# Kernel tuning notes

Hardware: AMD Instinct MI355X
Metric: run time of the kernel (lower is better)

## Reference

```python
import jax, jax.numpy as jnp
import numpy as np

D_MODEL = 2048
N_HEAD = 16
HEAD_DIM = D_MODEL // N_HEAD
SCALE = 1.0 / (HEAD_DIM ** 0.5)


def setup_inputs() -> dict:
    key = jax.random.key(0)
    kx, kq, kk, kv, ko = jax.random.split(key, 5)
    std = 1.0 / np.sqrt(D_MODEL)
    return {
        "x": jax.random.normal(kx, (2, 2048, D_MODEL), dtype=jnp.float32),
        "w_q": jax.random.normal(kq, (D_MODEL, D_MODEL), dtype=jnp.float32) * std,
        "w_k": jax.random.normal(kk, (D_MODEL, D_MODEL), dtype=jnp.float32) * std,
        "w_v": jax.random.normal(kv, (D_MODEL, D_MODEL), dtype=jnp.float32) * std,
        "w_o": jax.random.normal(ko, (D_MODEL, D_MODEL), dtype=jnp.float32) * std,
    }


def reference(x, w_q, w_k, w_v, w_o):
    b, s, d = x.shape
    # nn.Linear(d,d,bias=False): y = x @ W^T, weights stored [out, in]
    def proj(w):
        y = jnp.einsum("bsd,ed->bse", x, w)
        return y.reshape(b, s, N_HEAD, HEAD_DIM).transpose(0, 2, 1, 3)  # [b,h,s,hd]
    q, k, v = proj(w_q), proj(w_k), proj(w_v)
    scores = jnp.einsum("bhqd,bhkd->bhqk", q, k) * SCALE  # [b,h,s,s]
    probs = jax.nn.softmax(scores, axis=-1)
    attn = jnp.einsum("bhqk,bhkd->bhqd", probs, v)
    attn = attn.transpose(0, 2, 1, 3).reshape(b, s, d)
    return jnp.einsum("bsd,ed->bse", attn, w_o)
```

## Files before the change

### kernel.cpp

```cpp
#include <hip/hip_runtime.h>

#define D_MODEL 2048
#define SEQ 2048
#define BATCH 2
#define NH 16
#define HD 128
#define MTOT 4096
#define NQKV 6144
#define QSTRIDE 4096

static constexpr float SCALE_LOG2E = 0.08838834764831845f * 1.4426950408889634f;

typedef __bf16 bf16x8 __attribute__((ext_vector_type(8)));
typedef _Float16 f16x4 __attribute__((ext_vector_type(4)));
typedef float f32x4 __attribute__((ext_vector_type(4)));

__device__ inline unsigned short f2bf(float f) {
  unsigned int u = __builtin_bit_cast(unsigned int, f);
  u += 0x7fffu + ((u >> 16) & 1u);
  return (unsigned short)(u >> 16);
}

__device__ inline float bf2f(unsigned int u) {
  return __builtin_bit_cast(float, u << 16);
}

__device__ inline float fast_exp2(float x) {
#if __has_builtin(__builtin_amdgcn_exp2f)
  return __builtin_amdgcn_exp2f(x);
#else
  return exp2f(x);
#endif
}

__device__ inline unsigned int bperm(int srcLane, unsigned int v) {
  return (unsigned int)__builtin_amdgcn_ds_bpermute(srcLane << 2, (int)v);
}

__device__ inline void gload_lds16(const void* g, void* s) {
  __builtin_amdgcn_global_load_lds(
      (__attribute__((address_space(1))) void*)g,
      (__attribute__((address_space(3))) void*)s, 16, 0, 0);
}

#define BARX() __builtin_amdgcn_s_barrier()
#define PRIO(x) __builtin_amdgcn_s_setprio(x)
#define LGK0()                                              \
  do {                                                      \
    asm volatile("s_waitcnt lgkmcnt(0)" ::: "memory");      \
    __builtin_amdgcn_sched_barrier(0);                      \
  } while (0)
#define VMW(n) asm volatile("s_waitcnt vmcnt(" #n ")" ::: "memory")

__global__ __launch_bounds__(256) void cvt_all(
    const float* __restrict__ x, const float* __restrict__ wq,
    const float* __restrict__ wk, const float* __restrict__ wv,
    const float* __restrict__ wo, unsigned short* __restrict__ xb,
    unsigned short* __restrict__ wqkv, unsigned short* __restrict__ wob) {
  const int y = blockIdx.y;
  const float* src;
  unsigned short* dst;
  int n4;
  if (y == 0) { src = x; dst = xb; n4 = MTOT * D_MODEL / 4; }
  else if (y == 4) { src = wo; dst = wob; n4 = D_MODEL * D_MODEL / 4; }
  else {
    src = (y == 1) ? wq : (y == 2) ? wk : wv;
    dst = wqkv + (size_t)(y - 1) * D_MODEL * D_MODEL;
    n4 = D_MODEL * D_MODEL / 4;
  }
  int i = blockIdx.x * 256 + threadIdx.x;
  if (i < n4) {
    float4 v = ((const float4*)src)[i];
    ushort4 o;
    o.x = f2bf(v.x); o.y = f2bf(v.y); o.z = f2bf(v.z); o.w = f2bf(v.w);
    ((ushort4*)dst)[i] = o;
  }
}

__global__ __launch_bounds__(512, 2) void gemm_qk(
    const unsigned short* __restrict__ A, const unsigned short* __restrict__ B,
    unsigned short* __restrict__ QK) {
  extern __shared__ __align__(16) char smem[];
  const int tid = threadIdx.x;
  const int lane = tid & 63;
  const int wave = tid >> 6;
  const int quad = lane >> 4;
  const int l15 = lane & 15;
  const int bid = blockIdx.x;
  const int wgid = (bid & 7) * 32 + (bid >> 3);
  const int tm = wgid >> 4, tn = wgid & 15;
  const int m0 = tm * 256, n0 = tn * 256;
  const int wm = wave >> 2;
  const int wn = wave & 3;

  const unsigned short* Ag = A + (size_t)(m0 + wave * 8 + (lane >> 3)) * 2048 +
                             (((lane & 7) ^ (lane >> 3)) * 8);
  const unsigned short* Bg = B + (size_t)(n0 + wave * 8 + (lane >> 3)) * 2048 +
                             (((lane & 7) ^ (lane >> 3)) * 8);
  char* sd = smem + wave * 1024;

  const int arow0 = (wm * 128 + l15) * 128;
  const int brow0 = (wn * 64 + l15) * 128;
  const int sk0 = (quad ^ (l15 & 7)) * 16;
  const int sk1 = ((4 + quad) ^ (l15 & 7)) * 16;

  f32x4 acc[8][4] = {};
  bf16x8 a[4][2], bl[2][2], bh[2][2];

#define QSA(u, nb, ko) \
  gload_lds16(Ag + (size_t)(u) * 64 * 2048 + (ko), sd + (nb) * 65536 + (u) * 8192)
#define QSB(u, nb, ko) \
  gload_lds16(Bg + (size_t)(u) * 64 * 2048 + (ko), sd + (nb) * 65536 + 32768 + (u) * 8192)
#define QRA(mh, cb)                                                               \
  _Pragma("unroll") for (int mi = 0; mi < 4; mi++) {                              \
    a[mi][0] = *(const bf16x8*)(smem + (cb) * 65536 + arow0 + ((mh) * 64 + mi * 16) * 128 + sk0); \
    a[mi][1] = *(const bf16x8*)(smem + (cb) * 65536 + arow0 + ((mh) * 64 + mi * 16) * 128 + sk1); \
  }
#define QRB(dst, nh, cb)                                                          \
  _Pragma("unroll") for (int ni = 0; ni < 2; ni++) {                              \
    dst[ni][0] = *(const bf16x8*)(smem + (cb) * 65536 + 32768 + brow0 + ((nh) * 32 + ni * 16) * 128 + sk0); \
    dst[ni][1] = *(const bf16x8*)(smem + (cb) * 65536 + 32768 + brow0 + ((nh) * 32 + ni * 16) * 128 + sk1); \
  }
#define QMM(mh, bsrc, nh)                                                         \
  _Pragma("unroll") for (int mi = 0; mi < 4; mi++)                                \
  _Pragma("unroll") for (int ni = 0; ni < 2; ni++) {                              \
    acc[(mh) * 4 + mi][(nh) * 2 + ni] = __builtin_amdgcn_mfma_f32_16x16x32_bf16(  \
        a[mi][0], bsrc[ni][0], acc[(mh) * 4 + mi][(nh) * 2 + ni], 0, 0, 0);       \
    acc[(mh) * 4 + mi][(nh) * 2 + ni] = __builtin_amdgcn_mfma_f32_16x16x32_bf16(  \
        a[mi][1], bsrc[ni][1], acc[(mh) * 4 + mi][(nh) * 2 + ni], 0, 0, 0);       \
  }

  QSB(0, 0, 0); QSB(1, 0, 0); QSB(2, 0, 0); QSB(3, 0, 0);
  QSA(0, 0, 0); QSA(2, 0, 0); QSA(1, 0, 0); QSA(3, 0, 0);
  VMW(0);
  BARX();

#define QKTILE(t, cb, nb)                                                         \
  {                                                                               \
    const int ko = (((t) + 1) & 31) * 64;                                         \
                                                                         \
    QRA(0, cb); QRB(bl, 0, cb);                                                   \
    QSB(0, nb, ko); QSB(1, nb, ko);                                               \
    BARX(); LGK0(); PRIO(1); QMM(0, bl, 0); PRIO(0); BARX();                      \
                                                                         \
    QRB(bh, 1, cb);                                                               \
    QSB(2, nb, ko); QSB(3, nb, ko);                                               \
    BARX(); LGK0(); PRIO(1); QMM(0, bh, 1); PRIO(0); VMW(4); BARX();              \
                                                                         \
    QRA(1, cb);                                                                   \
    QSA(0, nb, ko); QSA(2, nb, ko);                                               \
    BARX(); LGK0(); PRIO(1); QMM(1, bl, 0); PRIO(0); BARX();                      \
                                                                         \
    QSA(1, nb, ko); QSA(3, nb, ko);                                               \
    PRIO(1); QMM(1, bh, 1); PRIO(0); VMW(2); BARX();                              \
  }

  for (int t = 0; t < 32; t += 2) {
    QKTILE(t, 0, 1);
    QKTILE(t + 1, 1, 0);
  }

#pragma unroll
  for (int mi = 0; mi < 8; mi++)
#pragma unroll
    for (int ni = 0; ni < 4; ni++) {
      const int mm = m0 + wm * 128 + mi * 16 + quad * 4;
      const int nn = n0 + wn * 64 + ni * 16 + l15;
#pragma unroll
      for (int r = 0; r < 4; r++)
        QK[(size_t)(mm + r) * QSTRIDE + nn] = f2bf(acc[mi][ni][r]);
    }
#undef QSA
#undef QSB
#undef QRA
#undef QRB
#undef QMM
#undef QKTILE
}

#define VCORE_BODY(Aptr, Bptr)                                                    \
  const int tid = threadIdx.x;                                                    \
  const int lane = tid & 63;                                                      \
  const int wave = tid >> 6;                                                      \
  const int quad = lane >> 4;                                                     \
  const int l15 = lane & 15;                                                      \
  const int bid = blockIdx.x;                                                     \
  const int wgid = (bid & 7) * 32 + (bid >> 3);                                   \
  const int tm = wgid >> 3, tn = wgid & 7;                                        \
  const int m0 = tm * 128, n0 = tn * 256;                                         \
  const int wm = wave >> 1;                                             \
  const int wn = wave & 1;                                              \
  const unsigned short* Ag = (Aptr) + (size_t)(m0 + wave * 8 + (lane >> 3)) * 2048 + \
                             (((lane & 7) ^ (lane >> 3)) * 8);                    \
  const unsigned short* Bg = (Bptr) + (size_t)(n0 + wave * 8 + (lane >> 3)) * 2048 + \
                             (((lane & 7) ^ (lane >> 3)) * 8);                    \
  char* sd = smem + wave * 1024;                                                  \
  const int arow0 = (wm * 32 + l15) * 128;                                        \
  const int brow0 = (wn * 128 + l15) * 128;                                       \
  const int sk0 = (quad ^ (l15 & 7)) * 16;                                        \
  const int sk1 = ((4 + quad) ^ (l15 & 7)) * 16;                                  \
  f32x4 acc[2][8] = {};                                                           \
  bf16x8 a[2][2], bl[4][2], bh[4][2];

#define VSA(u, nb, ko) \
  gload_lds16(Ag + (size_t)(u) * 64 * 2048 + (ko), sd + (nb) * 49152 + (u) * 8192)
#define VSB(u, nb, ko) \
  gload_lds16(Bg + (size_t)(u) * 64 * 2048 + (ko), sd + (nb) * 49152 + 16384 + (u) * 8192)
#define VRA(cb)                                                                   \
  _Pragma("unroll") for (int mi = 0; mi < 2; mi++) {                              \
    a[mi][0] = *(const bf16x8*)(smem + (cb) * 49152 + arow0 + mi * 2048 + sk0);   \
    a[mi][1] = *(const bf16x8*)(smem + (cb) * 49152 + arow0 + mi * 2048 + sk1);   \
  }
#define VRB(dst, nh, cb)                                                          \
  _Pragma("unroll") for (int ni = 0; ni < 4; ni++) {                              \
    dst[ni][0] = *(const bf16x8*)(smem + (cb) * 49152 + 16384 + brow0 + ((nh) * 64 + ni * 16) * 128 + sk0); \
    dst[ni][1] = *(const bf16x8*)(smem + (cb) * 49152 + 16384 + brow0 + ((nh) * 64 + ni * 16) * 128 + sk1); \
  }
#define VMM(bsrc, nh)                                                             \
  _Pragma("unroll") for (int mi = 0; mi < 2; mi++)                                \
  _Pragma("unroll") for (int ni = 0; ni < 4; ni++) {                              \
    acc[mi][(nh) * 4 + ni] = __builtin_amdgcn_mfma_f32_16x16x32_bf16(             \
        a[mi][0], bsrc[ni][0], acc[mi][(nh) * 4 + ni], 0, 0, 0);                  \
    acc[mi][(nh) * 4 + ni] = __builtin_amdgcn_mfma_f32_16x16x32_bf16(             \
        a[mi][1], bsrc[ni][1], acc[mi][(nh) * 4 + ni], 0, 0, 0);                  \
  }
#define VSTAGE6(nb, ko)                                                           \
  VSA(0, nb, ko); VSA(1, nb, ko); VSB(0, nb, ko);                                 \
  VSB(1, nb, ko); VSB(2, nb, ko); VSB(3, nb, ko);

#define VTILE(t, cb, nb)                                                          \
  {                                                                               \
    const int ko = (((t) + 2) & 31) * 64;                                         \
                                                                         \
    VRA(cb); VRB(bl, 0, cb);                                                      \
    VSA(0, nb, ko); VSA(1, nb, ko); VSB(0, nb, ko);                               \
    BARX(); LGK0(); PRIO(1); VMM(bl, 0); PRIO(0); BARX();                         \
                                                                         \
    VRB(bh, 1, cb);                                                               \
    VSB(1, nb, ko); VSB(2, nb, ko); VSB(3, nb, ko);                               \
    BARX(); LGK0(); PRIO(1); VMM(bh, 1); PRIO(0); VMW(6); BARX();                 \
  }

#define VCORE_LOOP()                                                              \
  VSTAGE6(0, 0);                                                                  \
  VSTAGE6(1, 64);                                                                 \
  VMW(6);                                                                         \
  BARX();                                                                         \
  for (int t = 0; t < 30; t += 3) {                                               \
    VTILE(t + 0, 0, 2);                                                           \
    VTILE(t + 1, 1, 0);                                                           \
    VTILE(t + 2, 2, 1);                                                           \
  }                                                                               \
  VTILE(30, 0, 2);                                                                \
  VTILE(31, 1, 0);

__global__ __launch_bounds__(512, 2) void gemm_v(
    const unsigned short* __restrict__ A, const unsigned short* __restrict__ B,
    unsigned short* __restrict__ Vt) {
  extern __shared__ __align__(16) char smem[];
  VCORE_BODY(A, B);
  VCORE_LOOP();

  VMW(0);
  BARX();
  unsigned short* T = (unsigned short*)smem;
  const int h0 = n0 >> 7;
  const int bb = m0 >> 11;
  const int sbase = m0 & (SEQ - 1);
#pragma unroll
  for (int mi = 0; mi < 2; mi++)
#pragma unroll
    for (int q = 0; q < 8; q++) {
      const int d = q * 16 + l15;
      const int slocal = wm * 32 + mi * 16 + quad * 4;
      ushort4 hv;
      hv.x = f2bf(acc[mi][q][0]);
      hv.y = f2bf(acc[mi][q][1]);
      hv.z = f2bf(acc[mi][q][2]);
      hv.w = f2bf(acc[mi][q][3]);
      *(ushort4*)(T + wn * 17408 + d * 136 + slocal) = hv;
    }
  BARX();
  const int hd2 = tid >> 8;
  const int d = (tid >> 1) & 127;
  const int sc = (tid & 1) * 64;
  const size_t vrow = ((size_t)((bb * NH + h0 + hd2) * HD + d)) * SEQ + sbase + sc;
#pragma unroll
  for (int j = 0; j < 8; j++) {
    float4 c4 = *(const float4*)(T + hd2 * 17408 + d * 136 + sc + j * 8);
    *(float4*)(Vt + vrow + j * 8) = c4;
  }
}

__global__ __launch_bounds__(512, 2) void gemm_out(
    const unsigned short* __restrict__ A, const unsigned short* __restrict__ B,
    float* __restrict__ C) {
  extern __shared__ __align__(16) char smem[];
  VCORE_BODY(A, B);
  VCORE_LOOP();

#pragma unroll
  for (int mi = 0; mi < 2; mi++)
#pragma unroll
    for (int q = 0; q < 8; q++) {
      const int mm = m0 + wm * 32 + mi * 16 + quad * 4;
      const int nn = n0 + wn * 128 + q * 16 + l15;
#pragma unroll
      for (int r = 0; r < 4; r++)
        C[(size_t)(mm + r) * D_MODEL + nn] = acc[mi][q][r];
    }
}

__global__ __launch_bounds__(256, 2) void flash_attn(
    const unsigned short* __restrict__ QK, const unsigned short* __restrict__ Vt,
    unsigned short* __restrict__ Og) {
  __shared__ __align__(16) unsigned short Ks[2][64 * 128];
  const int tid = threadIdx.x;
  const int lane = tid & 63;
  const int wave = tid >> 6;
  const int quad = lane >> 4;
  const int l15 = lane & 15;
  const int id = blockIdx.x;
  const int xr = id & 7;
  const int kk = id >> 3;
  const int bh = xr * 4 + (kk >> 4);
  const int b = bh >> 4, h = bh & 15;
  const int q0 = (kk & 15) * 128;

  const size_t kbase = (size_t)(b * SEQ) * QSTRIDE + D_MODEL + h * HD;
  const size_t vbase = (size_t)bh * HD * SEQ;

  bf16x8 qf[2][4];
#pragma unroll
  for (int t = 0; t < 2; t++)
#pragma unroll
    for (int kc = 0; kc < 4; kc++)
      qf[t][kc] = *(const bf16x8*)(QK + (size_t)(b * SEQ + q0 + wave * 32 + t * 16 + l15) * QSTRIDE +
                                   h * HD + kc * 32 + quad * 8);

  const unsigned short* kg[4];
  int klofs[4];
#pragma unroll
  for (int i = 0; i < 4; i++) {
    int krow = wave * 16 + i * 4 + quad;
    int kc_ = l15 ^ (i * 4 + quad);
    kg[i] = QK + kbase + (size_t)krow * QSTRIDE + kc_ * 8;
    klofs[i] = (wave * 16 + i * 4) * 128;
  }

  const unsigned short* vp[8];
#pragma unroll
  for (int jt = 0; jt < 8; jt++)
    vp[jt] = Vt + vbase + (size_t)(jt * 16 + l15) * SEQ + quad * 8;

#pragma unroll
  for (int i = 0; i < 4; i++) gload_lds16(kg[i], &Ks[0][klofs[i]]);
#pragma unroll
  for (int i = 0; i < 4; i++) kg[i] += 64 * QSTRIDE;
  VMW(0);
  __syncthreads();

  float lsum[2] = {0.f, 0.f};
  f32x4 Oa[2][8] = {};

  const int laA = l15 + 32 * (quad & 1);
  const int laB = laA + 16;
  const bool hi = quad >= 2;

  for (int it = 0; it < SEQ / 64; ++it) {
    const int cur = it & 1;
    if (it < SEQ / 64 - 1) {
#pragma unroll
      for (int i = 0; i < 4; i++) gload_lds16(kg[i], &Ks[cur ^ 1][klofs[i]]);
#pragma unroll
      for (int i = 0; i < 4; i++) kg[i] += 64 * QSTRIDE;
    }

    const unsigned short* kb = &Ks[cur][0];
    f32x4 sacc[2][4] = {};
    PRIO(1);
#pragma unroll
    for (int js = 0; js < 4; js++)
#pragma unroll
      for (int kc = 0; kc < 4; kc++) {
        bf16x8 kf = *(const bf16x8*)(kb + (js * 16 + l15) * 128 + (((kc * 4 + quad) ^ l15) * 8));
        sacc[0][js] = __builtin_amdgcn_mfma_f32_16x16x32_bf16(kf, qf[0][kc], sacc[0][js], 0, 0, 0);
        sacc[1][js] = __builtin_amdgcn_mfma_f32_16x16x32_bf16(kf, qf[1][kc], sacc[1][js], 0, 0, 0);
      }
    PRIO(0);

    unsigned int pw[2][4][2];
#pragma unroll
    for (int t = 0; t < 2; t++)
#pragma unroll
      for (int js = 0; js < 4; js++) {
        float p0 = fast_exp2(sacc[t][js][0] * SCALE_LOG2E);
        float p1 = fast_exp2(sacc[t][js][1] * SCALE_LOG2E);
        float p2 = fast_exp2(sacc[t][js][2] * SCALE_LOG2E);
        float p3 = fast_exp2(sacc[t][js][3] * SCALE_LOG2E);
        unsigned int b0 = f2bf(p0), b1 = f2bf(p1), b2 = f2bf(p2), b3 = f2bf(p3);
        pw[t][js][0] = b0 | (b1 << 16);
        pw[t][js][1] = b2 | (b3 << 16);
        lsum[t] += (bf2f(b0) + bf2f(b1)) + (bf2f(b2) + bf2f(b3));
      }

    bf16x8 pb8[2][2];
#pragma unroll
    for (int t = 0; t < 2; t++)
#pragma unroll
      for (int g = 0; g < 2; g++) {
        const int j0 = 2 * g, j1 = 2 * g + 1;
        unsigned int a0 = bperm(laA, pw[t][j0][0]), c0 = bperm(laA, pw[t][j1][0]);
        unsigned int a1 = bperm(laA, pw[t][j0][1]), c1 = bperm(laA, pw[t][j1][1]);
        unsigned int a2 = bperm(laB, pw[t][j0][0]), c2 = bperm(laB, pw[t][j1][0]);
        unsigned int a3 = bperm(laB, pw[t][j0][1]), c3 = bperm(laB, pw[t][j1][1]);
        uint4 u;
        u.x = hi ? c0 : a0;
        u.y = hi ? c1 : a1;
        u.z = hi ? c2 : a2;
        u.w = hi ? c3 : a3;
        pb8[t][g] = __builtin_bit_cast(bf16x8, u);
      }

    const int ko = it * 64;
    PRIO(1);
#pragma unroll
    for (int jt = 0; jt < 8; jt++) {
      bf16x8 v0 = *(const bf16x8*)(vp[jt] + ko);
      bf16x8 v1 = *(const bf16x8*)(vp[jt] + ko + 32);
      Oa[0][jt] = __builtin_amdgcn_mfma_f32_16x16x32_bf16(v0, pb8[0][0], Oa[0][jt], 0, 0, 0);
      Oa[1][jt] = __builtin_amdgcn_mfma_f32_16x16x32_bf16(v0, pb8[1][0], Oa[1][jt], 0, 0, 0);
      Oa[0][jt] = __builtin_amdgcn_mfma_f32_16x16x32_bf16(v1, pb8[0][1], Oa[0][jt], 0, 0, 0);
      Oa[1][jt] = __builtin_amdgcn_mfma_f32_16x16x32_bf16(v1, pb8[1][1], Oa[1][jt], 0, 0, 0);
    }
    PRIO(0);

    if (it < SEQ / 64 - 1) {
      VMW(0);
    }
    __syncthreads();
  }

  float inv[2];
#pragma unroll
  for (int t = 0; t < 2; t++) {
    float s = lsum[t];
    s += __shfl_xor(s, 16);
    s += __shfl_xor(s, 32);
    inv[t] = 1.0f / s;
  }

#pragma unroll
  for (int t = 0; t < 2; t++) {
    const size_t rowbase = (size_t)(b * SEQ + q0 + wave * 32 + t * 16 + l15) * D_MODEL + h * HD;
#pragma unroll
    for (int jt = 0; jt < 8; jt++) {
      ushort4 o;
      o.x = f2bf(Oa[t][jt][0] * inv[t]);
      o.y = f2bf(Oa[t][jt][1] * inv[t]);
      o.z = f2bf(Oa[t][jt][2] * inv[t]);
      o.w = f2bf(Oa[t][jt][3] * inv[t]);
      *(ushort4*)(Og + rowbase + jt * 16 + quad * 4) = o;
    }
  }
}

extern "C" void kernel_launch(void* const* d_in, const int* in_sizes, int n_in,
                              void* d_out, int out_size, void* d_ws, size_t ws_size,
                              hipStream_t stream) {
  const float* x = (const float*)d_in[0];
  const float* wq = (const float*)d_in[1];
  const float* wk = (const float*)d_in[2];
  const float* wv = (const float*)d_in[3];
  const float* wo = (const float*)d_in[4];
  float* out = (float*)d_out;
  char* ws = (char*)d_ws;
  const size_t MB = 1u << 20;
  if (ws_size < 96 * MB) return;

  unsigned short* xb = (unsigned short*)(ws);
  unsigned short* wqkv = (unsigned short*)(ws + 16 * MB);
  unsigned short* wob = (unsigned short*)(ws + 40 * MB);
  unsigned short* QKb = (unsigned short*)(ws + 48 * MB);
  unsigned short* Vtb = (unsigned short*)(ws + 80 * MB);
  unsigned short* Ab = xb;

  static int lds_set = 0;
  if (!lds_set) {
    hipFuncSetAttribute((const void*)gemm_qk,
                        hipFuncAttributeMaxDynamicSharedMemorySize, 131072);
    hipFuncSetAttribute((const void*)gemm_v,
                        hipFuncAttributeMaxDynamicSharedMemorySize, 147456);
    hipFuncSetAttribute((const void*)gemm_out,
                        hipFuncAttributeMaxDynamicSharedMemorySize, 147456);
    lds_set = 1;
  }

  cvt_all<<<dim3(8192, 5), 256, 0, stream>>>(x, wq, wk, wv, wo, xb, wqkv, wob);

  gemm_qk<<<256, 512, 131072, stream>>>(xb, wqkv, QKb);
  gemm_v<<<256, 512, 147456, stream>>>(xb, wqkv + (size_t)4096 * 2048, Vtb);

  flash_attn<<<512, 256, 0, stream>>>(QKb, Vtb, Ab);

  gemm_out<<<256, 512, 147456, stream>>>(Ab, wob, out);
}
```

Measured before the change: 423.7 us.

## Stage V tiles through double-buffered swizzled LDS in flash attention

```diff
diff --git a/kernel.cpp b/kernel.cpp
--- a/kernel.cpp
+++ b/kernel.cpp
@@ -12,7 +12,6 @@
 static constexpr float SCALE_LOG2E = 0.08838834764831845f * 1.4426950408889634f;
 
 typedef __bf16 bf16x8 __attribute__((ext_vector_type(8)));
-typedef _Float16 f16x4 __attribute__((ext_vector_type(4)));
 typedef float f32x4 __attribute__((ext_vector_type(4)));
 
 __device__ inline unsigned short f2bf(float f) {
@@ -315,6 +314,7 @@
     const unsigned short* __restrict__ QK, const unsigned short* __restrict__ Vt,
     unsigned short* __restrict__ Og) {
   __shared__ __align__(16) unsigned short Ks[2][64 * 128];
+  __shared__ __align__(16) unsigned short Vs[2][128 * 64];
   const int tid = threadIdx.x;
   const int lane = tid & 63;
   const int wave = tid >> 6;
@@ -348,15 +348,25 @@
     klofs[i] = (wave * 16 + i * 4) * 128;
   }
 
-  const unsigned short* vp[8];
-#pragma unroll
-  for (int jt = 0; jt < 8; jt++)
-    vp[jt] = Vt + vbase + (size_t)(jt * 16 + l15) * SEQ + quad * 8;
+  const unsigned short* vg[4];
+  int vlofs[4];
+#pragma unroll
+  for (int u = 0; u < 4; u++) {
+    int vrow = u * 32 + (tid >> 3);
+    int vslot = tid & 7;
+    int vchunk = vslot ^ (vrow & 7);
+    vg[u] = Vt + vbase + (size_t)vrow * SEQ + vchunk * 8;
+    vlofs[u] = vrow * 64 + vslot * 8;
+  }
 
 #pragma unroll
   for (int i = 0; i < 4; i++) gload_lds16(kg[i], &Ks[0][klofs[i]]);
 #pragma unroll
+  for (int u = 0; u < 4; u++) gload_lds16(vg[u], &Vs[0][vlofs[u]]);
+#pragma unroll
   for (int i = 0; i < 4; i++) kg[i] += 64 * QSTRIDE;
+#pragma unroll
+  for (int u = 0; u < 4; u++) vg[u] += 64;
   VMW(0);
   __syncthreads();
 
@@ -366,6 +376,8 @@
   const int laA = l15 + 32 * (quad & 1);
   const int laB = laA + 16;
   const bool hi = quad >= 2;
+  const int vsk0 = (quad ^ (l15 & 7)) * 8;
+  const int vsk1 = ((4 + quad) ^ (l15 & 7)) * 8;
 
   for (int it = 0; it < SEQ / 64; ++it) {
     const int cur = it & 1;
@@ -373,7 +385,11 @@
 #pragma unroll
       for (int i = 0; i < 4; i++) gload_lds16(kg[i], &Ks[cur ^ 1][klofs[i]]);
 #pragma unroll
+      for (int u = 0; u < 4; u++) gload_lds16(vg[u], &Vs[cur ^ 1][vlofs[u]]);
+#pragma unroll
       for (int i = 0; i < 4; i++) kg[i] += 64 * QSTRIDE;
+#pragma unroll
+      for (int u = 0; u < 4; u++) vg[u] += 64;
     }
 
     const unsigned short* kb = &Ks[cur][0];
@@ -422,12 +438,13 @@
         pb8[t][g] = __builtin_bit_cast(bf16x8, u);
       }
 
-    const int ko = it * 64;
+    const unsigned short* vb = &Vs[cur][0];
     PRIO(1);
 #pragma unroll
     for (int jt = 0; jt < 8; jt++) {
-      bf16x8 v0 = *(const bf16x8*)(vp[jt] + ko);
-      bf16x8 v1 = *(const bf16x8*)(vp[jt] + ko + 32);
+      const int vrow = (jt * 16 + l15) * 64;
+      bf16x8 v0 = *(const bf16x8*)(vb + vrow + vsk0);
+      bf16x8 v1 = *(const bf16x8*)(vb + vrow + vsk1);
       Oa[0][jt] = __builtin_amdgcn_mfma_f32_16x16x32_bf16(v0, pb8[0][0], Oa[0][jt], 0, 0, 0);
       Oa[1][jt] = __builtin_amdgcn_mfma_f32_16x16x32_bf16(v0, pb8[1][0], Oa[1][jt], 0, 0, 0);
       Oa[0][jt] = __builtin_amdgcn_mfma_f32_16x16x32_bf16(v1, pb8[0][1], Oa[0][jt], 0, 0, 0);
```

After: 363.2 us. -14.3%, faster.

## Stage V tiles in LDS, use 8 waves per flash block, fold scale into Q

Applied to the files above, without the earlier changes.

```diff
diff --git a/kernel.cpp b/kernel.cpp
--- a/kernel.cpp
+++ b/kernel.cpp
@@ -12,17 +12,12 @@
 static constexpr float SCALE_LOG2E = 0.08838834764831845f * 1.4426950408889634f;
 
 typedef __bf16 bf16x8 __attribute__((ext_vector_type(8)));
-typedef _Float16 f16x4 __attribute__((ext_vector_type(4)));
 typedef float f32x4 __attribute__((ext_vector_type(4)));
 
 __device__ inline unsigned short f2bf(float f) {
   unsigned int u = __builtin_bit_cast(unsigned int, f);
   u += 0x7fffu + ((u >> 16) & 1u);
   return (unsigned short)(u >> 16);
-}
-
-__device__ inline float bf2f(unsigned int u) {
-  return __builtin_bit_cast(float, u << 16);
 }
 
 __device__ inline float fast_exp2(float x) {
@@ -160,6 +155,7 @@
     QKTILE(t + 1, 1, 0);
   }
 
+  const float qs = (n0 < 2048) ? SCALE_LOG2E : 1.0f;
 #pragma unroll
   for (int mi = 0; mi < 8; mi++)
 #pragma unroll
@@ -168,7 +164,7 @@
       const int nn = n0 + wn * 64 + ni * 16 + l15;
 #pragma unroll
       for (int r = 0; r < 4; r++)
-        QK[(size_t)(mm + r) * QSTRIDE + nn] = f2bf(acc[mi][ni][r]);
+        QK[(size_t)(mm + r) * QSTRIDE + nn] = f2bf(acc[mi][ni][r] * qs);
     }
 #undef QSA
 #undef QSB
@@ -311,10 +307,11 @@
     }
 }
 
-__global__ __launch_bounds__(256, 2) void flash_attn(
+__global__ __launch_bounds__(512, 4) void flash_attn(
     const unsigned short* __restrict__ QK, const unsigned short* __restrict__ Vt,
     unsigned short* __restrict__ Og) {
   __shared__ __align__(16) unsigned short Ks[2][64 * 128];
+  __shared__ __align__(16) unsigned short Vs[2][128 * 64];
   const int tid = threadIdx.x;
   const int lane = tid & 63;
   const int wave = tid >> 6;
@@ -330,108 +327,111 @@
   const size_t kbase = (size_t)(b * SEQ) * QSTRIDE + D_MODEL + h * HD;
   const size_t vbase = (size_t)bh * HD * SEQ;
 
-  bf16x8 qf[2][4];
-#pragma unroll
-  for (int t = 0; t < 2; t++)
-#pragma unroll
-    for (int kc = 0; kc < 4; kc++)
-      qf[t][kc] = *(const bf16x8*)(QK + (size_t)(b * SEQ + q0 + wave * 32 + t * 16 + l15) * QSTRIDE +
-                                   h * HD + kc * 32 + quad * 8);
-
-  const unsigned short* kg[4];
-  int klofs[4];
-#pragma unroll
-  for (int i = 0; i < 4; i++) {
-    int krow = wave * 16 + i * 4 + quad;
-    int kc_ = l15 ^ (i * 4 + quad);
-    kg[i] = QK + kbase + (size_t)krow * QSTRIDE + kc_ * 8;
-    klofs[i] = (wave * 16 + i * 4) * 128;
-  }
-
-  const unsigned short* vp[8];
-#pragma unroll
-  for (int jt = 0; jt < 8; jt++)
-    vp[jt] = Vt + vbase + (size_t)(jt * 16 + l15) * SEQ + quad * 8;
-
-#pragma unroll
-  for (int i = 0; i < 4; i++) gload_lds16(kg[i], &Ks[0][klofs[i]]);
-#pragma unroll
-  for (int i = 0; i < 4; i++) kg[i] += 64 * QSTRIDE;
+  bf16x8 qf[4];
+#pragma unroll
+  for (int kc = 0; kc < 4; kc++)
+    qf[kc] = *(const bf16x8*)(QK + (size_t)(b * SEQ + q0 + wave * 16 + l15) * QSTRIDE +
+                              h * HD + kc * 32 + quad * 8);
+
+  const unsigned short* kg[2];
+  int klofs[2];
+#pragma unroll
+  for (int u = 0; u < 2; u++) {
+    const int krow = u * 32 + (tid >> 4);
+    const int chunk = (tid & 15) ^ (krow & 15);
+    kg[u] = QK + kbase + (size_t)krow * QSTRIDE + chunk * 8;
+    klofs[u] = u * 4096 + tid * 8;
+  }
+  const unsigned short* vg[2];
+  int vlofs[2];
+#pragma unroll
+  for (int u = 0; u < 2; u++) {
+    const int vrow = u * 64 + (tid >> 3);
+    const int chunk = (tid & 7) ^ (vrow & 7);
+    vg[u] = Vt + vbase + (size_t)vrow * SEQ + chunk * 8;
+    vlofs[u] = u * 4096 + tid * 8;
+  }
+
+#pragma unroll
+  for (int u = 0; u < 2; u++) gload_lds16(kg[u], &Ks[0][klofs[u]]);
+#pragma unroll
+  for (int u = 0; u < 2; u++) gload_lds16(vg[u], &Vs[0][vlofs[u]]);
+#pragma unroll
+  for (int u = 0; u < 2; u++) { kg[u] += 64 * QSTRIDE; vg[u] += 64; }
   VMW(0);
   __syncthreads();
 
-  float lsum[2] = {0.f, 0.f};
-  f32x4 Oa[2][8] = {};
+  float lsum = 0.f;
+  f32x4 Oa[8] = {};
 
   const int laA = l15 + 32 * (quad & 1);
   const int laB = laA + 16;
   const bool hi = quad >= 2;
+  const int vsk0 = (quad ^ (l15 & 7)) * 8;
+  const int vsk1 = ((4 + quad) ^ (l15 & 7)) * 8;
 
   for (int it = 0; it < SEQ / 64; ++it) {
     const int cur = it & 1;
     if (it < SEQ / 64 - 1) {
 #pragma unroll
-      for (int i = 0; i < 4; i++) gload_lds16(kg[i], &Ks[cur ^ 1][klofs[i]]);
-#pragma unroll
-      for (int i = 0; i < 4; i++) kg[i] += 64 * QSTRIDE;
+      for (int u = 0; u < 2; u++) gload_lds16(kg[u], &Ks[cur ^ 1][klofs[u]]);
+#pragma unroll
+      for (int u = 0; u < 2; u++) gload_lds16(vg[u], &Vs[cur ^ 1][vlofs[u]]);
+#pragma unroll
+      for (int u = 0; u < 2; u++) { kg[u] += 64 * QSTRIDE; vg[u] += 64; }
     }
 
     const unsigned short* kb = &Ks[cur][0];
-    f32x4 sacc[2][4] = {};
+    f32x4 sacc[4] = {};
     PRIO(1);
 #pragma unroll
     for (int js = 0; js < 4; js++)
 #pragma unroll
       for (int kc = 0; kc < 4; kc++) {
         bf16x8 kf = *(const bf16x8*)(kb + (js * 16 + l15) * 128 + (((kc * 4 + quad) ^ l15) * 8));
-        sacc[0][js] = __builtin_amdgcn_mfma_f32_16x16x32_bf16(kf, qf[0][kc], sacc[0][js], 0, 0, 0);
-        sacc[1][js] = __builtin_amdgcn_mfma_f32_16x16x32_bf16(kf, qf[1][kc], sacc[1][js], 0, 0, 0);
+        sacc[js] = __builtin_amdgcn_mfma_f32_16x16x32_bf16(kf, qf[kc], sacc[js], 0, 0, 0);
       }
     PRIO(0);
 
-    unsigned int pw[2][4][2];
-#pragma unroll
-    for (int t = 0; t < 2; t++)
-#pragma unroll
-      for (int js = 0; js < 4; js++) {
-        float p0 = fast_exp2(sacc[t][js][0] * SCALE_LOG2E);
-        float p1 = fast_exp2(sacc[t][js][1] * SCALE_LOG2E);
-        float p2 = fast_exp2(sacc[t][js][2] * SCALE_LOG2E);
-        float p3 = fast_exp2(sacc[t][js][3] * SCALE_LOG2E);
-        unsigned int b0 = f2bf(p0), b1 = f2bf(p1), b2 = f2bf(p2), b3 = f2bf(p3);
-        pw[t][js][0] = b0 | (b1 << 16);
-        pw[t][js][1] = b2 | (b3 << 16);
-        lsum[t] += (bf2f(b0) + bf2f(b1)) + (bf2f(b2) + bf2f(b3));
-      }
-
-    bf16x8 pb8[2][2];
-#pragma unroll
-    for (int t = 0; t < 2; t++)
-#pragma unroll
-      for (int g = 0; g < 2; g++) {
-        const int j0 = 2 * g, j1 = 2 * g + 1;
-        unsigned int a0 = bperm(laA, pw[t][j0][0]), c0 = bperm(laA, pw[t][j1][0]);
-        unsigned int a1 = bperm(laA, pw[t][j0][1]), c1 = bperm(laA, pw[t][j1][1]);
-        unsigned int a2 = bperm(laB, pw[t][j0][0]), c2 = bperm(laB, pw[t][j1][0]);
-        unsigned int a3 = bperm(laB, pw[t][j0][1]), c3 = bperm(laB, pw[t][j1][1]);
-        uint4 u;
-        u.x = hi ? c0 : a0;
-        u.y = hi ? c1 : a1;
-        u.z = hi ? c2 : a2;
-        u.w = hi ? c3 : a3;
-        pb8[t][g] = __builtin_bit_cast(bf16x8, u);
-      }
-
-    const int ko = it * 64;
+    unsigned int pw[4][2];
+#pragma unroll
+    for (int js = 0; js < 4; js++) {
+      __bf16 b0 = (__bf16)fast_exp2(sacc[js][0]);
+      __bf16 b1 = (__bf16)fast_exp2(sacc[js][1]);
+      __bf16 b2 = (__bf16)fast_exp2(sacc[js][2]);
+      __bf16 b3 = (__bf16)fast_exp2(sacc[js][3]);
+      lsum += ((float)b0 + (float)b1) + ((float)b2 + (float)b3);
+      pw[js][0] = (unsigned int)__builtin_bit_cast(unsigned short, b0) |
+                  ((unsigned int)__builtin_bit_cast(unsigned short, b1) << 16);
+      pw[js][1] = (unsigned int)__builtin_bit_cast(unsigned short, b2) |
+                  ((unsigned int)__builtin_bit_cast(unsigned short, b3) << 16);
+    }
+
+    bf16x8 pb8[2];
+#pragma unroll
+    for (int g = 0; g < 2; g++) {
+      const int j0 = 2 * g, j1 = 2 * g + 1;
+      unsigned int a0 = bperm(laA, pw[j0][0]), c0 = bperm(laA, pw[j1][0]);
+      unsigned int a1 = bperm(laA, pw[j0][1]), c1 = bperm(laA, pw[j1][1]);
+      unsigned int a2 = bperm(laB, pw[j0][0]), c2 = bperm(laB, pw[j1][0]);
+      unsigned int a3 = bperm(laB, pw[j0][1]), c3 = bperm(laB, pw[j1][1]);
+      uint4 u;
+      u.x = hi ? c0 : a0;
+      u.y = hi ? c1 : a1;
+      u.z = hi ? c2 : a2;
+      u.w = hi ? c3 : a3;
+      pb8[g] = __builtin_bit_cast(bf16x8, u);
+    }
+
+    const unsigned short* vb = &Vs[cur][0];
     PRIO(1);
 #pragma unroll
     for (int jt = 0; jt < 8; jt++) {
-      bf16x8 v0 = *(const bf16x8*)(vp[jt] + ko);
-      bf16x8 v1 = *(const bf16x8*)(vp[jt] + ko + 32);
-      Oa[0][jt] = __builtin_amdgcn_mfma_f32_16x16x32_bf16(v0, pb8[0][0], Oa[0][jt], 0, 0, 0);
-      Oa[1][jt] = __builtin_amdgcn_mfma_f32_16x16x32_bf16(v0, pb8[1][0], Oa[1][jt], 0, 0, 0);
-      Oa[0][jt] = __builtin_amdgcn_mfma_f32_16x16x32_bf16(v1, pb8[0][1], Oa[0][jt], 0, 0, 0);
-      Oa[1][jt] = __builtin_amdgcn_mfma_f32_16x16x32_bf16(v1, pb8[1][1], Oa[1][jt], 0, 0, 0);
+      const int vrow = (jt * 16 + l15) * 64;
+      bf16x8 v0 = *(const bf16x8*)(vb + vrow + vsk0);
+      bf16x8 v1 = *(const bf16x8*)(vb + vrow + vsk1);
+      Oa[jt] = __builtin_amdgcn_mfma_f32_16x16x32_bf16(v0, pb8[0], Oa[jt], 0, 0, 0);
+      Oa[jt] = __builtin_amdgcn_mfma_f32_16x16x32_bf16(v1, pb8[1], Oa[jt], 0, 0, 0);
     }
     PRIO(0);
 
@@ -441,27 +441,20 @@
     __syncthreads();
   }
 
-  float inv[2];
-#pragma unroll
-  for (int t = 0; t < 2; t++) {
-    float s = lsum[t];
-    s += __shfl_xor(s, 16);
-    s += __shfl_xor(s, 32);
-    inv[t] = 1.0f / s;
-  }
-
-#pragma unroll
-  for (int t = 0; t < 2; t++) {
-    const size_t rowbase = (size_t)(b * SEQ + q0 + wave * 32 + t * 16 + l15) * D_MODEL + h * HD;
-#pragma unroll
-    for (int jt = 0; jt < 8; jt++) {
-      ushort4 o;
-      o.x = f2bf(Oa[t][jt][0] * inv[t]);
-      o.y = f2bf(Oa[t][jt][1] * inv[t]);
-      o.z = f2bf(Oa[t][jt][2] * inv[t]);
-      o.w = f2bf(Oa[t][jt][3] * inv[t]);
-      *(ushort4*)(Og + rowbase + jt * 16 + quad * 4) = o;
-    }
+  float s = lsum;
+  s += __shfl_xor(s, 16);
+  s += __shfl_xor(s, 32);
+  const float inv = 1.0f / s;
+
+  const size_t rowbase = (size_t)(b * SEQ + q0 + wave * 16 + l15) * D_MODEL + h * HD;
+#pragma unroll
+  for (int jt = 0; jt < 8; jt++) {
+    ushort4 o;
+    o.x = f2bf(Oa[jt][0] * inv);
+    o.y = f2bf(Oa[jt][1] * inv);
+    o.z = f2bf(Oa[jt][2] * inv);
+    o.w = f2bf(Oa[jt][3] * inv);
+    *(ushort4*)(Og + rowbase + jt * 16 + quad * 4) = o;
   }
 }
 
@@ -501,7 +494,7 @@
   gemm_qk<<<256, 512, 131072, stream>>>(xb, wqkv, QKb);
   gemm_v<<<256, 512, 147456, stream>>>(xb, wqkv + (size_t)4096 * 2048, Vtb);
 
-  flash_attn<<<512, 256, 0, stream>>>(QKb, Vtb, Ab);
+  flash_attn<<<512, 512, 0, stream>>>(QKb, Vtb, Ab);
 
   gemm_out<<<256, 512, 147456, stream>>>(Ab, wob, out);
 }
```

Result: faster. 363.1 us (-14.3%).
